# Kernel tuning notes

Measured on AMD Instinct MI355X. Metric: run time of the kernel, lower is better.

Reference implementation:

```python
import jax, jax.numpy as jnp
import numpy as np

B, C, L = 8, 256, 4096
OC = C // 2  # out_channels default
EPS = 1e-5


def setup_inputs() -> dict:
    key = jax.random.key(0)
    ks = jax.random.split(key, 12)
    s_in = 1.0 / np.sqrt(C)   # conv1d default init scale (kaiming-uniform-ish)
    s_oc = 1.0 / np.sqrt(OC)
    return {
        "x": jax.random.normal(ks[0], (B, C, L), dtype=jnp.float32),
        "g_w": jax.random.uniform(ks[1], (OC, C), jnp.float32, -s_in, s_in),
        "g_b": jax.random.uniform(ks[2], (OC,), jnp.float32, -s_in, s_in),
        # theta/phi weights: nn.init.normal_(w, 0.02) -> mean 0.02, std 1
        "theta_w": 0.02 + jax.random.normal(ks[3], (OC, C), dtype=jnp.float32),
        "theta_b": jax.random.uniform(ks[4], (OC,), jnp.float32, -s_in, s_in),
        "phi_w": 0.02 + jax.random.normal(ks[5], (OC, C), dtype=jnp.float32),
        "phi_b": jax.random.uniform(ks[6], (OC,), jnp.float32, -s_in, s_in),
        "W_w": jax.random.uniform(ks[7], (C, OC), jnp.float32, -s_oc, s_oc),
        "W_b": jax.random.uniform(ks[8], (C,), jnp.float32, -s_oc, s_oc),
        # BN affine: init to zero in the original; use small random for a meaningful test
        "gamma": 0.1 * jax.random.normal(ks[9], (C,), dtype=jnp.float32),
        "beta": 0.1 * jax.random.normal(ks[10], (C,), dtype=jnp.float32),
    }


def reference(x, g_w, g_b, theta_w, theta_b, phi_w, phi_b, W_w, W_b, gamma, beta):
    # x: (b, c, l). 1x1 conv == per-position linear map over channels.
    g_x = jnp.einsum('oc,bcl->bol', g_w, x) + g_b[None, :, None]        # (b, oc, l)
    theta_x = jnp.einsum('oc,bcl->bol', theta_w, x) + theta_b[None, :, None]
    phi_x = jnp.einsum('oc,bcl->bol', phi_w, x) + phi_b[None, :, None]
    # f = theta^T phi : (b, l, l) quadratic score matrix (no softmax)
    f = jnp.einsum('bok,bom->bkm', theta_x, phi_x)
    N = f.shape[-1]
    # y = (f @ g^T) / N, returned in (b, oc, l) layout
    y = jnp.einsum('bkm,bom->bok', f, g_x) / N
    W_y = jnp.einsum('co,bol->bcl', W_w, y) + W_b[None, :, None]        # (b, c, l)
    # BatchNorm1d (training mode: batch statistics over (b, l), biased var)
    mean = jnp.mean(W_y, axis=(0, 2), keepdims=True)
    var = jnp.mean((W_y - mean) ** 2, axis=(0, 2), keepdims=True)
    W_y = (W_y - mean) * jax.lax.rsqrt(var + EPS)
    W_y = gamma[None, :, None] * W_y + beta[None, :, None]
    return W_y + x  # residual
```

## Files before the change

kernel.cpp:

```cpp
#include <hip/hip_runtime.h>
#include <hip/hip_bf16.h>

#define B_ 8
#define C_ 256
#define OC_ 128
#define L_ 4096
#define EPS_ 1e-5f
#define SPLITK 4

typedef unsigned short u16;
typedef __attribute__((ext_vector_type(4))) unsigned short u16x4;
typedef __attribute__((ext_vector_type(8))) unsigned short u16x8;
typedef __attribute__((ext_vector_type(4))) float f32x4;
typedef __attribute__((ext_vector_type(8))) short bf16x8;

__device__ inline u16 f2bf(float f) {
  union { __hip_bfloat16 h; u16 u; } v;
  v.h = __float2bfloat16(f);
  return v.u;
}
__device__ inline float bf2f(u16 u) {
  union { float f; unsigned u; } v;
  v.u = ((unsigned)u) << 16;
  return v.f;
}

__device__ inline void gload_lds16(const void* g, void* lds) {
  __builtin_amdgcn_global_load_lds(
      (const __attribute__((address_space(1))) unsigned int*)g,
      (__attribute__((address_space(3))) unsigned int*)lds, 16, 0, 0);
}

__global__ __launch_bounds__(256) void k_cvt(const float* __restrict__ x,
                                             u16* __restrict__ Xb,
                                             u16* __restrict__ XbT,
                                             float* __restrict__ spartial) {
  __shared__ u16 T[64][73];
  __shared__ float P[64][17];
  const int b = blockIdx.z, c0 = blockIdx.y * 64, l0 = blockIdx.x * 64;
  const int tid = threadIdx.x;
#pragma unroll
  for (int it = 0; it < 4; ++it) {
    int idx = it * 256 + tid;
    int row = idx >> 4;
    int col = (idx & 15) << 2;
    size_t gi = ((size_t)(b * C_ + c0 + row)) * L_ + l0 + col;
    float4 v = *(const float4*)(x + gi);
    u16 u0 = f2bf(v.x), u1 = f2bf(v.y), u2 = f2bf(v.z), u3 = f2bf(v.w);
    u16x4 u = {u0, u1, u2, u3};
    *(u16x4*)(Xb + gi) = u;
    T[row][col] = u0; T[row][col + 1] = u1; T[row][col + 2] = u2; T[row][col + 3] = u3;
    P[row][idx & 15] = v.x + v.y + v.z + v.w;
  }
  __syncthreads();
  if (tid < 64) {
    float acc = 0.f;
#pragma unroll
    for (int j = 0; j < 16; j++) acc += P[tid][j];
    spartial[(size_t)blockIdx.x * (B_ * C_) + b * C_ + c0 + tid] = acc;
  }
#pragma unroll
  for (int it = 0; it < 4; ++it) {
    int idx = it * 256 + tid;
    int lrow = idx >> 4;
    int ccol = (idx & 15) << 2;
    u16x4 u = {T[ccol][lrow], T[ccol + 1][lrow], T[ccol + 2][lrow], T[ccol + 3][lrow]};
    *(u16x4*)(XbT + ((size_t)b * L_ + l0 + lrow) * C_ + c0 + ccol) = u;
  }
}

__global__ __launch_bounds__(256) void k_xxt(const u16* __restrict__ Xb,
                                             float* __restrict__ Spart) {
  const int b = blockIdx.z, split = blockIdx.y;
  const int ti = blockIdx.x >> 2, tj = blockIdx.x & 3;
  __shared__ u16 lds[2][2][64 * 64];
  const int tid = threadIdx.x, lane = tid & 63;
  const int wid = tid >> 6, wr = wid >> 1, wc = wid & 1;
  const u16* Arows = Xb + ((size_t)b * C_ + ti * 64) * L_;
  const u16* Brows = Xb + ((size_t)b * C_ + tj * 64) * L_;
  const int k0 = split * (L_ / SPLITK);
  f32x4 acc[2][2] = {};

  auto STAGE = [&](int buf, int kt) {
#pragma unroll
    for (int ch = 0; ch < 2; ch++) {
      int d = ch * 4096 + tid * 16;
      int row = d >> 7;
      int kb = (d & 127) ^ ((row & 7) << 4);
      gload_lds16(Arows + (size_t)row * L_ + k0 + kt + (kb >> 1), (char*)lds[buf][0] + d);
      gload_lds16(Brows + (size_t)row * L_ + k0 + kt + (kb >> 1), (char*)lds[buf][1] + d);
    }
  };

  STAGE(0, 0);
  asm volatile("s_waitcnt vmcnt(0)" ::: "memory");
  __syncthreads();
  int cur = 0;
  for (int kt = 0; kt < L_ / SPLITK; kt += 64) {
    if (kt + 64 < L_ / SPLITK) STAGE(cur ^ 1, kt + 64);
#pragma unroll
    for (int kk = 0; kk < 2; kk++) {
      bf16x8 af[2], bfr[2];
#pragma unroll
      for (int m = 0; m < 2; m++) {
        int row = wr * 32 + m * 16 + (lane & 15);
        int kb = ((kk << 6) + ((lane >> 4) << 4)) ^ ((row & 7) << 4);
        af[m] = *(const bf16x8*)((const char*)lds[cur][0] + row * 128 + kb);
      }
#pragma unroll
      for (int n = 0; n < 2; n++) {
        int row = wc * 32 + n * 16 + (lane & 15);
        int kb = ((kk << 6) + ((lane >> 4) << 4)) ^ ((row & 7) << 4);
        bfr[n] = *(const bf16x8*)((const char*)lds[cur][1] + row * 128 + kb);
      }
#pragma unroll
      for (int m = 0; m < 2; m++)
#pragma unroll
        for (int n = 0; n < 2; n++)
          acc[m][n] = __builtin_amdgcn_mfma_f32_16x16x32_bf16(af[m], bfr[n], acc[m][n], 0, 0, 0);
    }
    asm volatile("s_waitcnt vmcnt(0)" ::: "memory");
    __syncthreads();
    cur ^= 1;
  }
  float* Sp = Spart + ((size_t)split * B_ + b) * C_ * C_;
#pragma unroll
  for (int m = 0; m < 2; m++)
#pragma unroll
    for (int n = 0; n < 2; n++) {
      int r0 = ti * 64 + wr * 32 + m * 16 + ((lane >> 4) << 2);
      int c0 = tj * 64 + wc * 32 + n * 16 + (lane & 15);
#pragma unroll
      for (int r = 0; r < 4; r++)
        Sp[(size_t)(r0 + r) * C_ + c0] = acc[m][n][r];
    }
}

__global__ __launch_bounds__(256) void k_sreduce(const float* __restrict__ Spart,
                                                 const float* __restrict__ spartial,
                                                 const float* __restrict__ g_w,
                                                 float* __restrict__ S,
                                                 u16* __restrict__ Sb,
                                                 float* __restrict__ s,
                                                 float* __restrict__ gwT) {
  const int bid = blockIdx.x, tid = threadIdx.x;
  if (bid < (B_ * C_ * C_) / 256) {
    size_t idx = (size_t)bid * 256 + tid;
    float acc = 0.f;
    for (int sp = 0; sp < SPLITK; sp++) acc += Spart[(size_t)sp * B_ * C_ * C_ + idx];
    S[idx] = acc;
    Sb[idx] = f2bf(acc);
  } else if (bid < (B_ * C_ * C_) / 256 + (B_ * C_) / 256) {
    int idx2 = (bid - (B_ * C_ * C_) / 256) * 256 + tid;
    float acc = 0.f;
#pragma unroll 8
    for (int i = 0; i < 64; i++) acc += spartial[(size_t)i * (B_ * C_) + idx2];
    s[idx2] = acc;
  } else {
    int t = bid - ((B_ * C_ * C_) / 256 + (B_ * C_) / 256);
    int o = t * 8 + (tid & 7);
    int cbase = (tid >> 3) * 8;
#pragma unroll
    for (int k = 0; k < 8; k++) {
      int c = cbase + k;
      gwT[c * OC_ + o] = g_w[o * C_ + c];
    }
  }
}

__global__ __launch_bounds__(256) void k_mid1(const float* __restrict__ S,
                                              const float* __restrict__ s,
                                              const float* __restrict__ phi_w,
                                              const float* __restrict__ phi_b,
                                              const float* __restrict__ gwT,
                                              const float* __restrict__ g_b,
                                              float* __restrict__ MT) {
  const int b = blockIdx.x >> 5, ot = blockIdx.x & 31;
  const int tid = threadIdx.x;
  __shared__ float pw[4][257], t2[4][257], sl[256], ps_s[4], pb_s[4], redw[4][4];
  sl[tid] = s[b * C_ + tid];
#pragma unroll
  for (int r = 0; r < 4; r++) pw[r][tid] = phi_w[(ot * 4 + r) * C_ + tid];
  if (tid < 4) pb_s[tid] = phi_b[ot * 4 + tid];
  __syncthreads();
  float acc4[4] = {};
  const float* Sbr = S + (size_t)b * C_ * C_;
#pragma unroll 4
  for (int cp = 0; cp < C_; cp++) {
    float sv = Sbr[(size_t)cp * C_ + tid];
#pragma unroll
    for (int r = 0; r < 4; r++) acc4[r] += pw[r][cp] * sv;
  }
  const int lane = tid & 63, w = tid >> 6;
#pragma unroll
  for (int r = 0; r < 4; r++) {
    float v = pw[r][tid] * sl[tid];
#pragma unroll
    for (int off = 1; off < 64; off <<= 1) v += __shfl_xor(v, off, 64);
    if (lane == 0) redw[w][r] = v;
  }
#pragma unroll
  for (int r = 0; r < 4; r++) t2[r][tid] = acc4[r] + pb_s[r] * sl[tid];
  __syncthreads();
  if (tid < 4) ps_s[tid] = redw[0][tid] + redw[1][tid] + redw[2][tid] + redw[3][tid];
  __syncthreads();
  const int o = tid & 127, half = tid >> 7;
  float m0 = 0.f, m1 = 0.f;
#pragma unroll 4
  for (int c = 0; c < C_; c++) {
    float gv = gwT[c * OC_ + o];
    m0 += t2[half * 2][c] * gv;
    m1 += t2[half * 2 + 1][c] * gv;
  }
  float gb = g_b[o];
  int r0 = half * 2;
  MT[((size_t)b * OC_ + o) * OC_ + ot * 4 + r0]     = m0 + (ps_s[r0] + (float)L_ * pb_s[r0]) * gb;
  MT[((size_t)b * OC_ + o) * OC_ + ot * 4 + r0 + 1] = m1 + (ps_s[r0 + 1] + (float)L_ * pb_s[r0 + 1]) * gb;
}

__global__ __launch_bounds__(256) void k_mid2(const float* __restrict__ MT,
                                              const float* __restrict__ W_w,
                                              const float* __restrict__ theta_w,
                                              const float* __restrict__ theta_b,
                                              const float* __restrict__ W_b,
                                              const float* __restrict__ s,
                                              u16* __restrict__ Qb,
                                              float* __restrict__ qv,
                                              float* __restrict__ qs_g,
                                              float* __restrict__ sum1) {
  const int b = blockIdx.x >> 6, ct = blockIdx.x & 63;
  const int c0 = ct * 4;
  const int tid = threadIdx.x;
  __shared__ float ww[4][OC_], u_s[4][OC_ + 2], s_l[C_], q_s[4], redq[4][4];
  s_l[tid] = s[b * C_ + tid];
#pragma unroll
  for (int i = tid; i < 4 * OC_; i += 256)
    ww[i >> 7][i & 127] = W_w[(c0 + (i >> 7)) * OC_ + (i & 127)];
  __syncthreads();
  const int op = tid & 127, rh = tid >> 7;
  float ua0 = 0.f, ua1 = 0.f;
  const float* MTb = MT + (size_t)b * OC_ * OC_;
#pragma unroll 4
  for (int o = 0; o < OC_; o++) {
    float mv = MTb[(size_t)o * OC_ + op];
    ua0 += ww[rh * 2][o] * mv;
    ua1 += ww[rh * 2 + 1][o] * mv;
  }
  u_s[rh * 2][op] = ua0 * (1.f / (float)L_);
  u_s[rh * 2 + 1][op] = ua1 * (1.f / (float)L_);
  __syncthreads();
  {
    const int r = tid >> 6, lane = tid & 63;
    float v = u_s[r][lane] * theta_b[lane] + u_s[r][lane + 64] * theta_b[lane + 64];
#pragma unroll
    for (int off = 1; off < 64; off <<= 1) v += __shfl_xor(v, off, 64);
    if (lane == 0) {
      float qval = v + W_b[c0 + r];
      q_s[r] = qval;
      qv[b * C_ + c0 + r] = qval;
    }
  }
  float qa[4] = {};
#pragma unroll 2
  for (int o = 0; o < OC_; o++) {
    float tv = theta_w[(size_t)o * C_ + tid];
#pragma unroll
    for (int r = 0; r < 4; r++) qa[r] += u_s[r][o] * tv;
  }
#pragma unroll
  for (int r = 0; r < 4; r++)
    Qb[((size_t)b * C_ + c0 + r) * C_ + tid] = f2bf(qa[r]);
  const int lane = tid & 63, w = tid >> 6;
#pragma unroll
  for (int r = 0; r < 4; r++) {
    float v = qa[r] * s_l[tid];
#pragma unroll
    for (int off = 1; off < 64; off <<= 1) v += __shfl_xor(v, off, 64);
    if (lane == 0) redq[w][r] = v;
  }
  __syncthreads();
  if (tid < 4) {
    float qs = redq[0][tid] + redq[1][tid] + redq[2][tid] + redq[3][tid];
    qs_g[b * C_ + c0 + tid] = qs;
    sum1[b * C_ + c0 + tid] = qs + (float)L_ * q_s[tid];
  }
}

__global__ __launch_bounds__(256) void k_ystat(const u16* __restrict__ Qb,
                                               const u16* __restrict__ Sb,
                                               float* __restrict__ e2part) {
  const int b = blockIdx.z;
  const int chs = blockIdx.y >> 1, ct = blockIdx.y & 1;
  const int ks = blockIdx.x;
  __shared__ u16 lds[2 * 128 * 64];
  __shared__ float e2s[128][2];
  const int tid = threadIdx.x, lane = tid & 63;
  const int wid = tid >> 6, wr = wid >> 1, wc = wid & 1;
  const u16* Abase = Qb + ((size_t)b * C_ + ct * 128) * C_;
  const u16* Bbase = Sb + ((size_t)b * C_ + chs * 128) * C_;
  const int k0 = ks * 64;
  f32x4 acc[4][4] = {};
#pragma unroll
  for (int ch = 0; ch < 4; ch++) {
    int d = ch * 4096 + tid * 16;
    int row = d >> 7;
    int kb = (d & 127) ^ ((row & 7) << 4);
    gload_lds16(Abase + (size_t)row * C_ + k0 + (kb >> 1), (char*)lds + d);
    gload_lds16(Bbase + (size_t)row * C_ + k0 + (kb >> 1), (char*)lds + 16384 + d);
  }
  asm volatile("s_waitcnt vmcnt(0)" ::: "memory");
  __syncthreads();
#pragma unroll
  for (int kk = 0; kk < 2; kk++) {
    bf16x8 af[4], bfr[4];
#pragma unroll
    for (int m = 0; m < 4; m++) {
      int row = wr * 64 + m * 16 + (lane & 15);
      int kb = ((kk << 6) + ((lane >> 4) << 4)) ^ ((row & 7) << 4);
      af[m] = *(const bf16x8*)((const char*)lds + row * 128 + kb);
    }
#pragma unroll
    for (int n = 0; n < 4; n++) {
      int row = wc * 64 + n * 16 + (lane & 15);
      int kb = ((kk << 6) + ((lane >> 4) << 4)) ^ ((row & 7) << 4);
      bfr[n] = *(const bf16x8*)((const char*)lds + 16384 + row * 128 + kb);
    }
#pragma unroll
    for (int m = 0; m < 4; m++)
#pragma unroll
      for (int n = 0; n < 4; n++)
        acc[m][n] = __builtin_amdgcn_mfma_f32_16x16x32_bf16(af[m], bfr[n], acc[m][n], 0, 0, 0);
  }
  float e2a[4][4];
#pragma unroll
  for (int m = 0; m < 4; m++)
#pragma unroll
    for (int r = 0; r < 4; r++) e2a[m][r] = 0.f;
#pragma unroll
  for (int m = 0; m < 4; m++)
#pragma unroll
    for (int n = 0; n < 4; n++) {
      int ch = chs * 128 + wc * 64 + n * 16 + (lane & 15);
#pragma unroll
      for (int r = 0; r < 4; r++) {
        int c_loc = wr * 64 + m * 16 + ((lane >> 4) << 2) + r;
        float q2 = bf2f(Qb[((size_t)b * C_ + ct * 128 + c_loc) * C_ + ch]);
        e2a[m][r] += acc[m][n][r] * q2;
      }
    }
#pragma unroll
  for (int m = 0; m < 4; m++)
#pragma unroll
    for (int r = 0; r < 4; r++) {
      float v = e2a[m][r];
      v += __shfl_xor(v, 1, 64);
      v += __shfl_xor(v, 2, 64);
      v += __shfl_xor(v, 4, 64);
      v += __shfl_xor(v, 8, 64);
      if ((lane & 15) == 0) {
        int c_loc = wr * 64 + m * 16 + ((lane >> 4) << 2) + r;
        e2s[c_loc][wc] = v;
      }
    }
  __syncthreads();
  if (tid < 128)
    e2part[(((size_t)chs * 4 + ks) * B_ + b) * C_ + ct * 128 + tid] =
        e2s[tid][0] + e2s[tid][1];
}

__global__ __launch_bounds__(256) void k_out(const u16* __restrict__ Qb,
                                             const float* __restrict__ qv,
                                             const float* __restrict__ qs_g,
                                             const float* __restrict__ sum1,
                                             const float* __restrict__ e2part,
                                             const float* __restrict__ gamma,
                                             const float* __restrict__ beta,
                                             const u16* __restrict__ XbT,
                                             float* __restrict__ out) {
  const int b = blockIdx.z, ct = blockIdx.y, lt = blockIdx.x;
  __shared__ u16 Albs[2][128 * 64];
  __shared__ u16 Blbs[2][128 * 64];
  __shared__ float gsc_s[128], qp_s[128];
  const int tid = threadIdx.x, lane = tid & 63;
  const int wid = tid >> 6, wr = wid >> 1, wc = wid & 1;
  if (tid < 128) {
    int c = ct * 128 + tid;
    float m_ = 0.f, e_ = 0.f;
#pragma unroll
    for (int bb = 0; bb < B_; bb++) {
      m_ += sum1[bb * C_ + c];
      float e2 = 0.f;
#pragma unroll
      for (int sl = 0; sl < 8; sl++) e2 += e2part[((size_t)sl * B_ + bb) * C_ + c];
      float qq = qv[bb * C_ + c], qs = qs_g[bb * C_ + c];
      e_ += e2 + 2.f * qq * qs + (float)L_ * qq * qq;
    }
    const float inv_n = 1.f / (float)(B_ * L_);
    m_ *= inv_n;
    e_ *= inv_n;
    float var = e_ - m_ * m_;
    float g = gamma[c] * rsqrtf(var + EPS_);
    gsc_s[tid] = g;
    qp_s[tid] = g * (qv[b * C_ + c] - m_) + beta[c];
  }
  __syncthreads();
  const u16* Bbase = XbT + ((size_t)b * L_ + lt * 128) * C_;
  f32x4 acc[4][4] = {};
  u16x4 regs[8];
  const int jr = (tid & 15) * 4;
  const int rb = tid >> 4;
  auto LOADA = [&](int k0) {
#pragma unroll
    for (int pass = 0; pass < 8; pass++) {
      int row = pass * 16 + rb;
      regs[pass] = *(const u16x4*)(Qb + ((size_t)b * C_ + ct * 128 + row) * C_ + k0 + jr);
    }
  };
  auto WRITEA = [&](int buf, int k0) {
#pragma unroll
    for (int pass = 0; pass < 8; pass++) {
      int row = pass * 16 + rb;
      float g = gsc_s[row];
      int c = ct * 128 + row;
      u16x4 h;
#pragma unroll
      for (int i = 0; i < 4; i++) {
        float a = g * bf2f(regs[pass][i]);
        if (k0 + jr + i == c) a += 1.f;
        h[i] = f2bf(a);
      }
      int byte = (jr * 2) ^ ((row & 7) << 4);
      *(u16x4*)((char*)Albs[buf] + row * 128 + byte) = h;
    }
  };
  auto STAGEB = [&](int buf, int k0) {
#pragma unroll
    for (int ch = 0; ch < 4; ch++) {
      int d = ch * 4096 + tid * 16;
      int row = d >> 7;
      int kb = (d & 127) ^ ((row & 7) << 4);
      gload_lds16(Bbase + (size_t)row * C_ + k0 + (kb >> 1), (char*)Blbs[buf] + d);
    }
  };
  LOADA(0);
  STAGEB(0, 0);
  asm volatile("s_waitcnt vmcnt(0)" ::: "memory");
  WRITEA(0, 0);
  __syncthreads();
  int cur = 0;
  for (int k0 = 0; k0 < C_; k0 += 64) {
    bool hasNext = (k0 + 64 < C_);
    if (hasNext) {
      STAGEB(cur ^ 1, k0 + 64);
      LOADA(k0 + 64);
    }
#pragma unroll
    for (int kk = 0; kk < 2; kk++) {
      bf16x8 af[4], bfr[4];
#pragma unroll
      for (int m = 0; m < 4; m++) {
        int row = wr * 64 + m * 16 + (lane & 15);
        int kb = ((kk << 6) + ((lane >> 4) << 4)) ^ ((row & 7) << 4);
        af[m] = *(const bf16x8*)((const char*)Albs[cur] + row * 128 + kb);
      }
#pragma unroll
      for (int n = 0; n < 4; n++) {
        int row = wc * 64 + n * 16 + (lane & 15);
        int kb = ((kk << 6) + ((lane >> 4) << 4)) ^ ((row & 7) << 4);
        bfr[n] = *(const bf16x8*)((const char*)Blbs[cur] + row * 128 + kb);
      }
#pragma unroll
      for (int m = 0; m < 4; m++)
#pragma unroll
        for (int n = 0; n < 4; n++)
          acc[m][n] = __builtin_amdgcn_mfma_f32_16x16x32_bf16(af[m], bfr[n], acc[m][n], 0, 0, 0);
    }
    if (hasNext) {
      asm volatile("s_waitcnt vmcnt(0)" ::: "memory");
      WRITEA(cur ^ 1, k0 + 64);
    }
    __syncthreads();
    cur ^= 1;
  }
#pragma unroll
  for (int m = 0; m < 4; m++)
#pragma unroll
    for (int n = 0; n < 4; n++) {
      int cl = wr * 64 + m * 16 + ((lane >> 4) << 2);
      int c = ct * 128 + cl;
      int l = lt * 128 + wc * 64 + n * 16 + (lane & 15);
#pragma unroll
      for (int r = 0; r < 4; r++) {
        size_t gi = ((size_t)b * C_ + c + r) * L_ + l;
        out[gi] = acc[m][n][r] + qp_s[cl + r];
      }
    }
}

extern "C" void kernel_launch(void* const* d_in, const int* in_sizes, int n_in,
                              void* d_out, int out_size, void* d_ws, size_t ws_size,
                              hipStream_t stream) {
  const float* x       = (const float*)d_in[0];
  const float* g_w     = (const float*)d_in[1];
  const float* g_b     = (const float*)d_in[2];
  const float* theta_w = (const float*)d_in[3];
  const float* theta_b = (const float*)d_in[4];
  const float* phi_w   = (const float*)d_in[5];
  const float* phi_b   = (const float*)d_in[6];
  const float* W_w     = (const float*)d_in[7];
  const float* W_b     = (const float*)d_in[8];
  const float* gamma   = (const float*)d_in[9];
  const float* beta    = (const float*)d_in[10];
  float* out = (float*)d_out;

  float* ws = (float*)d_ws;
  size_t off = 0;
  float* Spart    = ws + off; off += (size_t)SPLITK * B_ * C_ * C_;
  float* S        = ws + off; off += (size_t)B_ * C_ * C_;
  float* spartial = ws + off; off += (size_t)B_ * C_ * 64;
  float* s_       = ws + off; off += B_ * C_;
  float* gwT      = ws + off; off += C_ * OC_;
  float* MT       = ws + off; off += (size_t)B_ * OC_ * OC_;
  float* qv       = ws + off; off += B_ * C_;
  float* qs_g     = ws + off; off += B_ * C_;
  float* sum1     = ws + off; off += B_ * C_;
  float* e2part   = ws + off; off += 8 * B_ * C_;
  u16* Sb  = (u16*)(ws + off); off += (size_t)B_ * C_ * C_ / 2;
  u16* Qb  = (u16*)(ws + off); off += (size_t)B_ * C_ * C_ / 2;
  u16* Xb  = (u16*)(ws + off); off += (size_t)B_ * C_ * L_ / 2;
  u16* XbT = (u16*)(ws + off); off += (size_t)B_ * C_ * L_ / 2;

  k_cvt<<<dim3(L_ / 64, C_ / 64, B_), 256, 0, stream>>>(x, Xb, XbT, spartial);
  k_xxt<<<dim3(16, SPLITK, B_), 256, 0, stream>>>(Xb, Spart);
  k_sreduce<<<(B_ * C_ * C_) / 256 + (B_ * C_) / 256 + 16, 256, 0, stream>>>(
      Spart, spartial, g_w, S, Sb, s_, gwT);
  k_mid1<<<B_ * 32, 256, 0, stream>>>(S, s_, phi_w, phi_b, gwT, g_b, MT);
  k_mid2<<<B_ * 64, 256, 0, stream>>>(MT, W_w, theta_w, theta_b, W_b, s_,
                                      Qb, qv, qs_g, sum1);
  k_ystat<<<dim3(4, 4, B_), 256, 0, stream>>>(Qb, Sb, e2part);
  k_out<<<dim3(L_ / 128, C_ / 128, B_), 256, 0, stream>>>(
      Qb, qv, qs_g, sum1, e2part, gamma, beta, XbT, out);
}
```

Measured before the change: 121.0 us.

## Exploit Gram symmetry in XX^T, fuse y-stat into mid2, swizzle block order

After: 121.6 us. No clear change (+0.5%).

```diff
diff --git a/kernel.cpp b/kernel.cpp
--- a/kernel.cpp
+++ b/kernel.cpp
@@ -6,7 +6,7 @@
 #define OC_ 128
 #define L_ 4096
 #define EPS_ 1e-5f
-#define SPLITK 4
+#define SPLITK 8
 
 typedef unsigned short u16;
 typedef __attribute__((ext_vector_type(4))) unsigned short u16x4;
@@ -71,8 +71,14 @@
 
 __global__ __launch_bounds__(256) void k_xxt(const u16* __restrict__ Xb,
                                              float* __restrict__ Spart) {
-  const int b = blockIdx.z, split = blockIdx.y;
-  const int ti = blockIdx.x >> 2, tj = blockIdx.x & 3;
+  int flat = blockIdx.x + 10 * (blockIdx.y + SPLITK * blockIdx.z);
+  int w = (flat & 7) * 80 + (flat >> 3);
+  const int bx = w % 10;
+  const int split = (w / 10) & 7;
+  const int b = w / 80;
+  const int TIa[10] = {0, 0, 0, 0, 1, 1, 1, 2, 2, 3};
+  const int TJa[10] = {0, 1, 2, 3, 1, 2, 3, 2, 3, 3};
+  const int ti = TIa[bx], tj = TJa[bx];
   __shared__ u16 lds[2][2][64 * 64];
   const int tid = threadIdx.x, lane = tid & 63;
   const int wid = tid >> 6, wr = wid >> 1, wc = wid & 1;
@@ -134,13 +140,33 @@
       for (int r = 0; r < 4; r++)
         Sp[(size_t)(r0 + r) * C_ + c0] = acc[m][n][r];
     }
+  if (ti != tj) {
+    float* TtF = (float*)lds;
+#pragma unroll
+    for (int m = 0; m < 2; m++)
+#pragma unroll
+      for (int n = 0; n < 2; n++) {
+        int cl = wc * 32 + n * 16 + (lane & 15);
+        int rl = wr * 32 + m * 16 + ((lane >> 4) << 2);
+#pragma unroll
+        for (int r = 0; r < 4; r++) TtF[cl * 65 + rl + r] = acc[m][n][r];
+      }
+    __syncthreads();
+#pragma unroll
+    for (int it = 0; it < 4; ++it) {
+      int idx = it * 256 + tid;
+      int cl = idx >> 4;
+      int r4 = (idx & 15) << 2;
+      *(float4*)(Sp + (size_t)(tj * 64 + cl) * C_ + ti * 64 + r4) =
+          *(float4*)(TtF + cl * 65 + r4);
+    }
+  }
 }
 
 __global__ __launch_bounds__(256) void k_sreduce(const float* __restrict__ Spart,
                                                  const float* __restrict__ spartial,
                                                  const float* __restrict__ g_w,
                                                  float* __restrict__ S,
-                                                 u16* __restrict__ Sb,
                                                  float* __restrict__ s,
                                                  float* __restrict__ gwT) {
   const int bid = blockIdx.x, tid = threadIdx.x;
@@ -149,7 +175,6 @@
     float acc = 0.f;
     for (int sp = 0; sp < SPLITK; sp++) acc += Spart[(size_t)sp * B_ * C_ * C_ + idx];
     S[idx] = acc;
-    Sb[idx] = f2bf(acc);
   } else if (bid < (B_ * C_ * C_) / 256 + (B_ * C_) / 256) {
     int idx2 = (bid - (B_ * C_ * C_) / 256) * 256 + tid;
     float acc = 0.f;
@@ -175,7 +200,8 @@
                                               const float* __restrict__ gwT,
                                               const float* __restrict__ g_b,
                                               float* __restrict__ MT) {
-  const int b = blockIdx.x >> 5, ot = blockIdx.x & 31;
+  int w = (blockIdx.x & 7) * 32 + (blockIdx.x >> 3);
+  const int b = w >> 5, ot = w & 31;
   const int tid = threadIdx.x;
   __shared__ float pw[4][257], t2[4][257], sl[256], ps_s[4], pb_s[4], redw[4][4];
   sl[tid] = s[b * C_ + tid];
@@ -191,13 +217,13 @@
 #pragma unroll
     for (int r = 0; r < 4; r++) acc4[r] += pw[r][cp] * sv;
   }
-  const int lane = tid & 63, w = tid >> 6;
+  const int lane = tid & 63, wv = tid >> 6;
 #pragma unroll
   for (int r = 0; r < 4; r++) {
     float v = pw[r][tid] * sl[tid];
 #pragma unroll
     for (int off = 1; off < 64; off <<= 1) v += __shfl_xor(v, off, 64);
-    if (lane == 0) redw[w][r] = v;
+    if (lane == 0) redw[wv][r] = v;
   }
 #pragma unroll
   for (int r = 0; r < 4; r++) t2[r][tid] = acc4[r] + pb_s[r] * sl[tid];
@@ -224,14 +250,18 @@
                                               const float* __restrict__ theta_b,
                                               const float* __restrict__ W_b,
                                               const float* __restrict__ s,
+                                              const float* __restrict__ S,
                                               u16* __restrict__ Qb,
                                               float* __restrict__ qv,
                                               float* __restrict__ qs_g,
-                                              float* __restrict__ sum1) {
-  const int b = blockIdx.x >> 6, ct = blockIdx.x & 63;
+                                              float* __restrict__ sum1,
+                                              float* __restrict__ e2sum) {
+  int wsw = (blockIdx.x & 7) * 64 + (blockIdx.x >> 3);
+  const int b = wsw >> 6, ct = wsw & 63;
   const int c0 = ct * 4;
   const int tid = threadIdx.x;
-  __shared__ float ww[4][OC_], u_s[4][OC_ + 2], s_l[C_], q_s[4], redq[4][4];
+  __shared__ float ww[4][OC_], u_s[4][OC_ + 2], s_l[C_], q_s[4], redq[4][4], rede[4][4];
+  __shared__ float qt[4][C_];
   s_l[tid] = s[b * C_ + tid];
 #pragma unroll
   for (int i = tid; i < 4 * OC_; i += 256)
@@ -246,8 +276,8 @@
     ua0 += ww[rh * 2][o] * mv;
     ua1 += ww[rh * 2 + 1][o] * mv;
   }
-  u_s[rh * 2][op] = ua0 * (1.f / (float)L_);
-  u_s[rh * 2 + 1][op] = ua1 * (1.f / (float)L_);
+  u_s[rh * 2][op] = ua0 * (1.0f / (float)L_);
+  u_s[rh * 2 + 1][op] = ua1 * (1.0f / (float)L_);
   __syncthreads();
   {
     const int r = tid >> 6, lane = tid & 63;
@@ -267,16 +297,21 @@
 #pragma unroll
     for (int r = 0; r < 4; r++) qa[r] += u_s[r][o] * tv;
   }
-#pragma unroll
-  for (int r = 0; r < 4; r++)
-    Qb[((size_t)b * C_ + c0 + r) * C_ + tid] = f2bf(qa[r]);
-  const int lane = tid & 63, w = tid >> 6;
+  float qr[4];
 #pragma unroll
   for (int r = 0; r < 4; r++) {
-    float v = qa[r] * s_l[tid];
+    u16 h = f2bf(qa[r]);
+    Qb[((size_t)b * C_ + c0 + r) * C_ + tid] = h;
+    qr[r] = bf2f(h);
+    qt[r][tid] = qr[r];
+  }
+  const int lane = tid & 63, wv = tid >> 6;
+#pragma unroll
+  for (int r = 0; r < 4; r++) {
+    float v = qr[r] * s_l[tid];
 #pragma unroll
     for (int off = 1; off < 64; off <<= 1) v += __shfl_xor(v, off, 64);
-    if (lane == 0) redq[w][r] = v;
+    if (lane == 0) redq[wv][r] = v;
   }
   __syncthreads();
   if (tid < 4) {
@@ -284,100 +319,38 @@
     qs_g[b * C_ + c0 + tid] = qs;
     sum1[b * C_ + c0 + tid] = qs + (float)L_ * q_s[tid];
   }
-}
-
-__global__ __launch_bounds__(256) void k_ystat(const u16* __restrict__ Qb,
-                                               const u16* __restrict__ Sb,
-                                               float* __restrict__ e2part) {
-  const int b = blockIdx.z;
-  const int chs = blockIdx.y >> 1, ct = blockIdx.y & 1;
-  const int ks = blockIdx.x;
-  __shared__ u16 lds[2 * 128 * 64];
-  __shared__ float e2s[128][2];
-  const int tid = threadIdx.x, lane = tid & 63;
-  const int wid = tid >> 6, wr = wid >> 1, wc = wid & 1;
-  const u16* Abase = Qb + ((size_t)b * C_ + ct * 128) * C_;
-  const u16* Bbase = Sb + ((size_t)b * C_ + chs * 128) * C_;
-  const int k0 = ks * 64;
-  f32x4 acc[4][4] = {};
-#pragma unroll
-  for (int ch = 0; ch < 4; ch++) {
-    int d = ch * 4096 + tid * 16;
-    int row = d >> 7;
-    int kb = (d & 127) ^ ((row & 7) << 4);
-    gload_lds16(Abase + (size_t)row * C_ + k0 + (kb >> 1), (char*)lds + d);
-    gload_lds16(Bbase + (size_t)row * C_ + k0 + (kb >> 1), (char*)lds + 16384 + d);
-  }
-  asm volatile("s_waitcnt vmcnt(0)" ::: "memory");
-  __syncthreads();
-#pragma unroll
-  for (int kk = 0; kk < 2; kk++) {
-    bf16x8 af[4], bfr[4];
-#pragma unroll
-    for (int m = 0; m < 4; m++) {
-      int row = wr * 64 + m * 16 + (lane & 15);
-      int kb = ((kk << 6) + ((lane >> 4) << 4)) ^ ((row & 7) << 4);
-      af[m] = *(const bf16x8*)((const char*)lds + row * 128 + kb);
-    }
-#pragma unroll
-    for (int n = 0; n < 4; n++) {
-      int row = wc * 64 + n * 16 + (lane & 15);
-      int kb = ((kk << 6) + ((lane >> 4) << 4)) ^ ((row & 7) << 4);
-      bfr[n] = *(const bf16x8*)((const char*)lds + 16384 + row * 128 + kb);
-    }
-#pragma unroll
-    for (int m = 0; m < 4; m++)
-#pragma unroll
-      for (int n = 0; n < 4; n++)
-        acc[m][n] = __builtin_amdgcn_mfma_f32_16x16x32_bf16(af[m], bfr[n], acc[m][n], 0, 0, 0);
-  }
-  float e2a[4][4];
-#pragma unroll
-  for (int m = 0; m < 4; m++)
-#pragma unroll
-    for (int r = 0; r < 4; r++) e2a[m][r] = 0.f;
-#pragma unroll
-  for (int m = 0; m < 4; m++)
-#pragma unroll
-    for (int n = 0; n < 4; n++) {
-      int ch = chs * 128 + wc * 64 + n * 16 + (lane & 15);
-#pragma unroll
-      for (int r = 0; r < 4; r++) {
-        int c_loc = wr * 64 + m * 16 + ((lane >> 4) << 2) + r;
-        float q2 = bf2f(Qb[((size_t)b * C_ + ct * 128 + c_loc) * C_ + ch]);
-        e2a[m][r] += acc[m][n][r] * q2;
-      }
-    }
-#pragma unroll
-  for (int m = 0; m < 4; m++)
-#pragma unroll
-    for (int r = 0; r < 4; r++) {
-      float v = e2a[m][r];
-      v += __shfl_xor(v, 1, 64);
-      v += __shfl_xor(v, 2, 64);
-      v += __shfl_xor(v, 4, 64);
-      v += __shfl_xor(v, 8, 64);
-      if ((lane & 15) == 0) {
-        int c_loc = wr * 64 + m * 16 + ((lane >> 4) << 2) + r;
-        e2s[c_loc][wc] = v;
-      }
-    }
-  __syncthreads();
-  if (tid < 128)
-    e2part[(((size_t)chs * 4 + ks) * B_ + b) * C_ + ct * 128 + tid] =
-        e2s[tid][0] + e2s[tid][1];
+  float yv[4] = {};
+  const float* Sbp = S + (size_t)b * C_ * C_;
+#pragma unroll 4
+  for (int cp = 0; cp < C_; cp++) {
+    float sv = Sbp[(size_t)cp * C_ + tid];
+#pragma unroll
+    for (int r = 0; r < 4; r++) yv[r] += qt[r][cp] * sv;
+  }
+#pragma unroll
+  for (int r = 0; r < 4; r++) {
+    float v = yv[r] * qt[r][tid];
+#pragma unroll
+    for (int off = 1; off < 64; off <<= 1) v += __shfl_xor(v, off, 64);
+    if (lane == 0) rede[wv][r] = v;
+  }
+  __syncthreads();
+  if (tid < 4)
+    e2sum[b * C_ + c0 + tid] = rede[0][tid] + rede[1][tid] + rede[2][tid] + rede[3][tid];
 }
 
 __global__ __launch_bounds__(256) void k_out(const u16* __restrict__ Qb,
                                              const float* __restrict__ qv,
                                              const float* __restrict__ qs_g,
                                              const float* __restrict__ sum1,
-                                             const float* __restrict__ e2part,
+                                             const float* __restrict__ e2sum,
                                              const float* __restrict__ gamma,
                                              const float* __restrict__ beta,
                                              const u16* __restrict__ XbT,
                                              float* __restrict__ out) {
-  const int b = blockIdx.z, ct = blockIdx.y, lt = blockIdx.x;
+  int flat = blockIdx.x + (L_ / 128) * (blockIdx.y + (C_ / 128) * blockIdx.z);
+  int wsw = (flat & 7) * 64 + (flat >> 3);
+  const int lt = wsw & 31, ct = (wsw >> 5) & 1, b = wsw >> 6;
   __shared__ u16 Albs[2][128 * 64];
   __shared__ u16 Blbs[2][128 * 64];
   __shared__ float gsc_s[128], qp_s[128];
@@ -389,11 +362,8 @@
 #pragma unroll
     for (int bb = 0; bb < B_; bb++) {
       m_ += sum1[bb * C_ + c];
-      float e2 = 0.f;
-#pragma unroll
-      for (int sl = 0; sl < 8; sl++) e2 += e2part[((size_t)sl * B_ + bb) * C_ + c];
       float qq = qv[bb * C_ + c], qs = qs_g[bb * C_ + c];
-      e_ += e2 + 2.f * qq * qs + (float)L_ * qq * qq;
+      e_ += e2sum[bb * C_ + c] + 2.f * qq * qs + (float)L_ * qq * qq;
     }
     const float inv_n = 1.f / (float)(B_ * L_);
     m_ *= inv_n;
@@ -524,20 +494,18 @@
   float* qv       = ws + off; off += B_ * C_;
   float* qs_g     = ws + off; off += B_ * C_;
   float* sum1     = ws + off; off += B_ * C_;
-  float* e2part   = ws + off; off += 8 * B_ * C_;
-  u16* Sb  = (u16*)(ws + off); off += (size_t)B_ * C_ * C_ / 2;
+  float* e2sum    = ws + off; off += B_ * C_;
   u16* Qb  = (u16*)(ws + off); off += (size_t)B_ * C_ * C_ / 2;
   u16* Xb  = (u16*)(ws + off); off += (size_t)B_ * C_ * L_ / 2;
   u16* XbT = (u16*)(ws + off); off += (size_t)B_ * C_ * L_ / 2;
 
   k_cvt<<<dim3(L_ / 64, C_ / 64, B_), 256, 0, stream>>>(x, Xb, XbT, spartial);
-  k_xxt<<<dim3(16, SPLITK, B_), 256, 0, stream>>>(Xb, Spart);
+  k_xxt<<<dim3(10, SPLITK, B_), 256, 0, stream>>>(Xb, Spart);
   k_sreduce<<<(B_ * C_ * C_) / 256 + (B_ * C_) / 256 + 16, 256, 0, stream>>>(
-      Spart, spartial, g_w, S, Sb, s_, gwT);
+      Spart, spartial, g_w, S, s_, gwT);
   k_mid1<<<B_ * 32, 256, 0, stream>>>(S, s_, phi_w, phi_b, gwT, g_b, MT);
-  k_mid2<<<B_ * 64, 256, 0, stream>>>(MT, W_w, theta_w, theta_b, W_b, s_,
-                                      Qb, qv, qs_g, sum1);
-  k_ystat<<<dim3(4, 4, B_), 256, 0, stream>>>(Qb, Sb, e2part);
+  k_mid2<<<B_ * 64, 256, 0, stream>>>(MT, W_w, theta_w, theta_b, W_b, s_, S,
+                                      Qb, qv, qs_g, sum1, e2sum);
   k_out<<<dim3(L_ / 128, C_ / 128, B_), 256, 0, stream>>>(
-      Qb, qv, qs_g, sum1, e2part, gamma, beta, XbT, out);
-}
+      Qb, qv, qs_g, sum1, e2sum, gamma, beta, XbT, out);
+}
```
